# Optimization experiments

Hardware: AMD Instinct MI355X
Metric: run time of the kernel (lower is better)

Reference implementation:

```python
import jax, jax.numpy as jnp
import numpy as np

# Model hyperparameters (from __init__)
SIGMA = 0.2
LAMBDA_0 = 1.0
LAMBDA_INF = 0.1
LAMBDA_DECAY = 0.01
MU_J = 0.0
SIGMA_J = 0.3
TOTAL_STEPS = 10000
KAPPA = float(np.exp(MU_J + 0.5 * SIGMA_J ** 2) - 1.0)  # E[e^Y - 1]

# Simulation dims (simulate_path args)
T_TOTAL = 1.0
N_STEPS = 2048
N_PATHS = 32768
DT = T_TOTAL / N_STEPS


def _jump_intensity(t):
    # lambda(t) = lambda_inf + (lambda_0 - lambda_inf) * exp(-decay * t)
    # (t/total_steps * total_steps cancels in the original code)
    return LAMBDA_INF + (LAMBDA_0 - LAMBDA_INF) * jnp.exp(-LAMBDA_DECAY * t)


def setup_inputs() -> dict:
    key = jax.random.key(0)
    k1, k2, k3 = jax.random.split(key, 3)
    # Per-step time-varying Poisson rate for jump counts
    t = jnp.arange(N_STEPS, dtype=jnp.float32) * DT  # (n_steps,)
    lam_dt = _jump_intensity(t) * DT                  # (n_steps,)
    n_jumps = jax.random.poisson(k3, lam_dt[:, None], shape=(N_STEPS, N_PATHS)).astype(jnp.int32)
    return {
        "S0": jnp.ones((1,), dtype=jnp.float32),                         # initial price
        "z_diff": jax.random.normal(k1, (N_STEPS, N_PATHS), jnp.float32),  # Brownian increments / sqrt(dt)
        "z_jump": jax.random.normal(k2, (N_STEPS, N_PATHS), jnp.float32),  # jump-sum normals
        "n_jumps": n_jumps,                                              # Poisson jump counts
    }


def reference(S0, z_diff, z_jump, n_jumps):
    dtype = z_diff.dtype
    t = jnp.arange(N_STEPS, dtype=dtype) * DT          # (n_steps,)
    lam = _jump_intensity(t)[:, None]                   # (n_steps, 1)
    # Sum of n_jumps iid N(mu_J, sigma_J^2) jumps == N(n*mu_J, n*sigma_J^2)
    nj = n_jumps.astype(dtype)
    jump_sizes = nj * MU_J + jnp.sqrt(nj) * SIGMA_J * z_jump
    drift = (0.0 - lam * KAPPA) * DT
    diffusion = SIGMA * jnp.asarray(np.sqrt(DT), dtype) * z_diff
    log_ret = drift + diffusion + jump_sizes            # (n_steps, n_paths)
    log_paths = jnp.cumsum(log_ret, axis=0)             # (n_steps, n_paths)
    log_paths = jnp.concatenate([jnp.zeros((1, log_ret.shape[1]), dtype), log_paths], axis=0)
    paths = (S0[0] * jnp.exp(log_paths)).T              # (n_paths, n_steps + 1)
    return paths
```

## Files before the change

kernel.cpp:

```cpp
#include <hip/hip_runtime.h>
#include <math.h>


#define N_STEPS 2048
#define N_PATHS 32768
#define ROW (N_STEPS + 1)

#define NWAVES 16
#define SUB 8
#define TILE_S (NWAVES * SUB)
#define NTILES (N_STEPS / TILE_S)

#define DT_F 0.00048828125f
#define C_DIFF_F 0.004419417382415922f
#define KAPPA_F 0.046027859908717f
#define ND_F (-4.8828125e-6f)

__device__ __forceinline__ void lds_barrier() {
    asm volatile("s_waitcnt lgkmcnt(0)" ::: "memory");
    __builtin_amdgcn_s_barrier();
}

__global__ __launch_bounds__(1024, 8) void merton_paths_kernel(
    const float* __restrict__ S0,
    const float* __restrict__ z_diff,
    const float* __restrict__ z_jump,
    const int* __restrict__ n_jumps,
    float* __restrict__ out) {
    const int tid  = threadIdx.x;
    const int lane = tid & 63;
    const int w    = tid >> 6;
    const int pbase = blockIdx.x * 64;
    const int p     = pbase + lane;
    const float s0  = S0[0];

    __shared__ float stage[2][64][TILE_S + 1];
    __shared__ float ws[NWAVES][64];

    const float r = __expf(ND_F);

    if (w == 0) out[p * ROW] = s0;

    float zd[SUB], zj[SUB], val[SUB];
    int   nj[SUB];

    {
        int idx = (w * SUB) * N_PATHS + p;
#pragma unroll
        for (int i = 0; i < SUB; ++i) {
            zd[i] = z_diff[idx];
            zj[i] = z_jump[idx];
            nj[i] = n_jumps[idx];
            idx += N_PATHS;
        }
        float e = __expf(ND_F * (float)(w * SUB));
#pragma unroll
        for (int i = 0; i < SUB; ++i) {
            float lam = 0.1f + 0.9f * e;
            e *= r;
            val[i] = (-(lam * KAPPA_F) * DT_F + C_DIFF_F * zd[i])
                   + sqrtf((float)nj[i]) * 0.3f * zj[i];
        }
    }

    float carry = 0.0f;

    for (int t = 0; t < NTILES; ++t) {
        const int tn = (t + 1 < NTILES) ? (t + 1) : 0;
        {
            int idx = (tn * TILE_S + w * SUB) * N_PATHS + p;
#pragma unroll
            for (int i = 0; i < SUB; ++i) {
                zd[i] = z_diff[idx];
                zj[i] = z_jump[idx];
                nj[i] = n_jumps[idx];
                idx += N_PATHS;
            }
        }

        float acc = 0.0f;
#pragma unroll
        for (int i = 0; i < SUB; ++i) { acc += val[i]; val[i] = acc; }
        ws[w][lane] = acc;
        lds_barrier();

        float pre = carry, tot = 0.0f;
#pragma unroll
        for (int ww = 0; ww < NWAVES; ++ww) {
            float v = ws[ww][lane];
            pre += (ww < w) ? v : 0.0f;
            tot += v;
        }
        carry += tot;

        const int buf = t & 1;
#pragma unroll
        for (int i = 0; i < SUB; ++i)
            stage[buf][lane][w * SUB + i] = s0 * __expf(pre + val[i]);
        lds_barrier();

        {
            float* obase = out + pbase * ROW + 1 + t * TILE_S;
#pragma unroll
            for (int k = 0; k < 4; ++k) {
                int rr = w * 4 + k;
                float* orow = obase + rr * ROW;
                orow[lane]      = stage[buf][rr][lane];
                orow[lane + 64] = stage[buf][rr][lane + 64];
            }
        }

        float e = __expf(ND_F * (float)(tn * TILE_S + w * SUB));
#pragma unroll
        for (int i = 0; i < SUB; ++i) {
            float lam = 0.1f + 0.9f * e;
            e *= r;
            val[i] = (-(lam * KAPPA_F) * DT_F + C_DIFF_F * zd[i])
                   + sqrtf((float)nj[i]) * 0.3f * zj[i];
        }
    }
}

extern "C" void kernel_launch(void* const* d_in, const int* in_sizes, int n_in,
                              void* d_out, int out_size, void* d_ws, size_t ws_size,
                              hipStream_t stream) {
    const float* S0      = (const float*)d_in[0];
    const float* z_diff  = (const float*)d_in[1];
    const float* z_jump  = (const float*)d_in[2];
    const int*   n_jumps = (const int*)d_in[3];
    float* out = (float*)d_out;

    dim3 block(1024);
    dim3 grid(N_PATHS / 64);
    hipLaunchKernelGGL(merton_paths_kernel, grid, block, 0, stream,
                       S0, z_diff, z_jump, n_jumps, out);
}
```

Before: 843.6 us.

## Process two paths per thread with vectorized float2 loads and 128-path blocks

Each thread now handles two adjacent paths, loading inputs as float2/int2 so global reads become 8-byte accesses, and each block covers 128 paths. The staging layout is transposed so each lane writes step-major columns and the readout remaps path rows. The previous register prefetch of the next tile is removed, so loads are issued at the start of each iteration. Launch bounds are relaxed to 4 blocks per CU to fit the doubled register footprint, trading some latency hiding for wider memory transactions.

```diff
diff --git a/kernel.cpp b/kernel.cpp
--- a/kernel.cpp
+++ b/kernel.cpp
@@ -5,11 +5,14 @@
 #define N_STEPS 2048
 #define N_PATHS 32768
 #define ROW (N_STEPS + 1)
+#define HALF (N_PATHS / 2)
 
 #define NWAVES 16
 #define SUB 8
 #define TILE_S (NWAVES * SUB)
 #define NTILES (N_STEPS / TILE_S)
+#define PPB 128
+#define STRIDE 129
 
 #define DT_F 0.00048828125f
 #define C_DIFF_F 0.004419417382415922f
@@ -21,7 +24,7 @@
     __builtin_amdgcn_s_barrier();
 }
 
-__global__ __launch_bounds__(1024, 8) void merton_paths_kernel(
+__global__ __launch_bounds__(1024, 4) void merton_paths_kernel(
     const float* __restrict__ S0,
     const float* __restrict__ z_diff,
     const float* __restrict__ z_jump,
@@ -30,93 +33,80 @@
     const int tid  = threadIdx.x;
     const int lane = tid & 63;
     const int w    = tid >> 6;
-    const int pbase = blockIdx.x * 64;
-    const int p     = pbase + lane;
-    const float s0  = S0[0];
+    const int pbase = blockIdx.x * PPB;
 
-    __shared__ float stage[2][64][TILE_S + 1];
-    __shared__ float ws[NWAVES][64];
+    const float price0 = S0[0];
+    const float2* zd2 = (const float2*)z_diff;
+    const float2* zj2 = (const float2*)z_jump;
+    const int2*   nj2 = (const int2*)n_jumps;
+
+    __shared__ float  stage[2][TILE_S][STRIDE];
+    __shared__ float2 ws2[NWAVES][64];
+
+    if (tid < PPB) out[(pbase + tid) * ROW] = price0;
 
     const float r = __expf(ND_F);
+    const int pidx = (pbase >> 1) + lane;
 
-    if (w == 0) out[p * ROW] = s0;
+    float carry0 = 0.0f, carry1 = 0.0f;
 
-    float zd[SUB], zj[SUB], val[SUB];
-    int   nj[SUB];
+    for (int t = 0; t < NTILES; ++t) {
+        const int step0 = t * TILE_S + w * SUB;
 
-    {
-        int idx = (w * SUB) * N_PATHS + p;
+        float2 zd[SUB], zj[SUB]; int2 nj[SUB];
+        {
+            int base = step0 * HALF + pidx;
 #pragma unroll
-        for (int i = 0; i < SUB; ++i) {
-            zd[i] = z_diff[idx];
-            zj[i] = z_jump[idx];
-            nj[i] = n_jumps[idx];
-            idx += N_PATHS;
+            for (int i = 0; i < SUB; ++i) {
+                zd[i] = zd2[base];
+                zj[i] = zj2[base];
+                nj[i] = nj2[base];
+                base += HALF;
+            }
         }
-        float e = __expf(ND_F * (float)(w * SUB));
+
+        float e = __expf(ND_F * (float)step0);
+        float a0 = 0.0f, a1 = 0.0f;
+        float c0[SUB], c1[SUB];
 #pragma unroll
         for (int i = 0; i < SUB; ++i) {
             float lam = 0.1f + 0.9f * e;
             e *= r;
-            val[i] = (-(lam * KAPPA_F) * DT_F + C_DIFF_F * zd[i])
-                   + sqrtf((float)nj[i]) * 0.3f * zj[i];
+            float drift = -(lam * KAPPA_F) * DT_F;
+            a0 += drift + C_DIFF_F * zd[i].x + sqrtf((float)nj[i].x) * 0.3f * zj[i].x;
+            a1 += drift + C_DIFF_F * zd[i].y + sqrtf((float)nj[i].y) * 0.3f * zj[i].y;
+            c0[i] = a0; c1[i] = a1;
         }
-    }
-
-    float carry = 0.0f;
-
-    for (int t = 0; t < NTILES; ++t) {
-        const int tn = (t + 1 < NTILES) ? (t + 1) : 0;
-        {
-            int idx = (tn * TILE_S + w * SUB) * N_PATHS + p;
-#pragma unroll
-            for (int i = 0; i < SUB; ++i) {
-                zd[i] = z_diff[idx];
-                zj[i] = z_jump[idx];
-                nj[i] = n_jumps[idx];
-                idx += N_PATHS;
-            }
-        }
-
-        float acc = 0.0f;
-#pragma unroll
-        for (int i = 0; i < SUB; ++i) { acc += val[i]; val[i] = acc; }
-        ws[w][lane] = acc;
+        ws2[w][lane] = make_float2(a0, a1);
         lds_barrier();
 
-        float pre = carry, tot = 0.0f;
+        float pre0 = carry0, pre1 = carry1, tot0 = 0.0f, tot1 = 0.0f;
 #pragma unroll
         for (int ww = 0; ww < NWAVES; ++ww) {
-            float v = ws[ww][lane];
-            pre += (ww < w) ? v : 0.0f;
-            tot += v;
+            float2 v = ws2[ww][lane];
+            if (ww < w) { pre0 += v.x; pre1 += v.y; }
+            tot0 += v.x; tot1 += v.y;
         }
-        carry += tot;
+        carry0 += tot0; carry1 += tot1;
 
         const int buf = t & 1;
 #pragma unroll
-        for (int i = 0; i < SUB; ++i)
-            stage[buf][lane][w * SUB + i] = s0 * __expf(pre + val[i]);
+        for (int i = 0; i < SUB; ++i) {
+            stage[buf][w * SUB + i][lane]      = price0 * __expf(pre0 + c0[i]);
+            stage[buf][w * SUB + i][lane + 64] = price0 * __expf(pre1 + c1[i]);
+        }
         lds_barrier();
 
         {
             float* obase = out + pbase * ROW + 1 + t * TILE_S;
 #pragma unroll
-            for (int k = 0; k < 4; ++k) {
-                int rr = w * 4 + k;
+            for (int k = 0; k < 8; ++k) {
+                int rr = w * 8 + k;
+                int col = (rr >> 1) + ((rr & 1) << 6);
                 float* orow = obase + rr * ROW;
-                orow[lane]      = stage[buf][rr][lane];
-                orow[lane + 64] = stage[buf][rr][lane + 64];
+                orow[lane]      = stage[buf][lane][col];
+                orow[lane + 64] = stage[buf][lane + 64][col];
             }
-        }
-
-        float e = __expf(ND_F * (float)(tn * TILE_S + w * SUB));
-#pragma unroll
-        for (int i = 0; i < SUB; ++i) {
-            float lam = 0.1f + 0.9f * e;
-            e *= r;
-            val[i] = (-(lam * KAPPA_F) * DT_F + C_DIFF_F * zd[i])
-                   + sqrtf((float)nj[i]) * 0.3f * zj[i];
         }
     }
 }
@@ -131,7 +121,7 @@
     float* out = (float*)d_out;
 
     dim3 block(1024);
-    dim3 grid(N_PATHS / 64);
+    dim3 grid(N_PATHS / PPB);
     hipLaunchKernelGGL(merton_paths_kernel, grid, block, 0, stream,
                        S0, z_diff, z_jump, n_jumps, out);
 }
```

Result: no change. 844.3 us (+0.1%).
